# Optimization experiments

Measured on AMD Instinct MI355X. Metric: run time of the kernel, lower is better.

The kernel has to match this reference:

```python
import jax, jax.numpy as jnp
import numpy as np

HIDDEN = 2048
QUANTILES = 16
BATCH = 8192
HALF = HIDDEN // 2


def setup_inputs() -> dict:
    key = jax.random.key(0)
    kx, k1, kb1, k2 = jax.random.split(key, 4)
    x = jax.random.normal(kx, (BATCH, HIDDEN), dtype=jnp.float32)
    # Stacked per-head params: head q computes Linear(H->H/2) -> GELU -> Linear(H/2->1)
    # PyTorch Linear default init ~ U(-1/sqrt(fan_in), 1/sqrt(fan_in)); last layer kaiming-normal, bias 0.
    lim1 = 1.0 / np.sqrt(HIDDEN)
    W1 = jax.random.uniform(k1, (QUANTILES, HIDDEN, HALF), minval=-lim1, maxval=lim1, dtype=jnp.float32)
    b1 = jax.random.uniform(kb1, (QUANTILES, HALF), minval=-lim1, maxval=lim1, dtype=jnp.float32)
    # kaiming_normal fan_in, linear nonlinearity -> std = 1/sqrt(fan_in)
    W2 = jax.random.normal(k2, (QUANTILES, HALF), dtype=jnp.float32) / np.sqrt(HALF)
    b2 = jnp.zeros((QUANTILES,), dtype=jnp.float32)
    return {"x": x, "W1": W1, "b1": b1, "W2": W2, "b2": b2}


def reference(x, W1, b1, W2, b2):
    # Batched over all quantile heads: one grouped GEMM + fused GELU + grouped GEMV.
    # h: [batch, quantiles, half]
    h = jnp.einsum('bh,qhk->bqk', x, W1) + b1[None, :, :]
    h = jax.nn.gelu(h, approximate=False)  # torch nn.GELU() default = exact erf GELU
    # out: [batch, quantiles]
    out = jnp.einsum('bqk,qk->bq', h, W2) + b2[None, :]
    return out
```

## Files before the change

### kernel.cpp

```cpp
#include <hip/hip_runtime.h>

#define HIDDEN 2048
#define QUANT  16
#define BATCH  8192
#define HALFD  1024

typedef _Float16 half8  __attribute__((ext_vector_type(8)));
typedef float    floatx16 __attribute__((ext_vector_type(16)));

__device__ __forceinline__ void load_lds16(const void* gptr, void* lptr) {
  __builtin_amdgcn_global_load_lds(
      (const __attribute__((address_space(1))) void*)gptr,
      (__attribute__((address_space(3))) void*)lptr, 16, 0, 0);
}

__device__ __forceinline__ float gelu_exact(float v) {
  const float z  = 0.7071067811865476f * v;
  const float az = fabsf(z);
  const float t  = __builtin_amdgcn_rcpf(1.0f + 0.3275911f * az);
  const float p  = t * (0.254829592f +
                   t * (-0.284496736f +
                   t * (1.421413741f +
                   t * (-1.453152027f +
                   t * 1.061405429f))));
  float er = 1.0f - p * __expf(-az * az);
  er = copysignf(er, z);
  return 0.5f * v * (1.0f + er);
}

__global__ __launch_bounds__(256) void convert_x_kernel(const float* __restrict__ x,
                                                        _Float16* __restrict__ xh) {
  const int i = (blockIdx.x * 256 + threadIdx.x) * 8;
  const float4 a = *(const float4*)(x + i);
  const float4 b = *(const float4*)(x + i + 4);
  half8 h;
  h[0] = (_Float16)a.x; h[1] = (_Float16)a.y; h[2] = (_Float16)a.z; h[3] = (_Float16)a.w;
  h[4] = (_Float16)b.x; h[5] = (_Float16)b.y; h[6] = (_Float16)b.z; h[7] = (_Float16)b.w;
  *(half8*)(xh + i) = h;
}

__global__ __launch_bounds__(256) void transpose_w1_kernel(const float* __restrict__ W1,
                                                           _Float16* __restrict__ W1T) {
  __shared__ float tile[64][33];
  const int q  = blockIdx.z;
  const int h0 = blockIdx.y * 64;
  const int n0 = blockIdx.x * 32;
  const float* src = W1 + (size_t)q * HIDDEN * HALFD;
  _Float16*    dst = W1T + (size_t)q * HALFD * HIDDEN;
  const int t  = threadIdx.x;
  const int lr = t >> 3;
  const int lc = (t & 7) * 4;
  #pragma unroll
  for (int j = 0; j < 2; ++j) {
    const float4 v = *(const float4*)(src + (size_t)(h0 + lr + 32 * j) * HALFD + n0 + lc);
    tile[lr + 32 * j][lc + 0] = v.x;
    tile[lr + 32 * j][lc + 1] = v.y;
    tile[lr + 32 * j][lc + 2] = v.z;
    tile[lr + 32 * j][lc + 3] = v.w;
  }
  __syncthreads();
  const int sn = t >> 3;
  const int sh = (t & 7) * 8;
  half8 v;
  #pragma unroll
  for (int c = 0; c < 8; ++c) v[c] = (_Float16)tile[sh + c][sn];
  *(half8*)(dst + (size_t)(n0 + sn) * HIDDEN + h0 + sh) = v;
}

__global__ __launch_bounds__(256) void init_out_kernel(float* __restrict__ out,
                                                       const float* __restrict__ b2) {
  const int i = blockIdx.x * 256 + threadIdx.x;
  out[i] = b2[i & (QUANT - 1)];
}

__global__ __launch_bounds__(256, 4) void qhead_gemm_kernel(
    const _Float16* __restrict__ A,
    const _Float16* __restrict__ BT,
    const float* __restrict__ b1,
    const float* __restrict__ W2,
    float* __restrict__ out) {
  __shared__ _Float16 As[128 * 64];
  __shared__ _Float16 Bs[128 * 64];

  const int tid  = threadIdx.x;
  const int lane = tid & 63;
  const int wave = tid >> 6;
  const int wm = wave >> 1, wn = wave & 1;
  const int r31 = lane & 31, l5 = lane >> 5, lx = lane & 7;

  const int m0 = blockIdx.y << 7;
  const int q  = blockIdx.x >> 3;
  const int n0 = (blockIdx.x & 7) << 7;

  const _Float16* Ablk = A + (size_t)m0 * HIDDEN;
  const _Float16* Bblk = BT + ((size_t)q * HALFD + n0) * HIDDEN;

  const int row_t = tid >> 3;
  const int gx = (((tid & 7) ^ (row_t & 7)) << 3);
  const _Float16* agp = Ablk + (size_t)row_t * HIDDEN + gx;
  const _Float16* bgp = Bblk + (size_t)row_t * HIDDEN + gx;
  _Float16* alp = &As[tid * 8];
  _Float16* blp = &Bs[tid * 8];

  int aoff[2], boff[2];
  #pragma unroll
  for (int f = 0; f < 2; ++f) {
    aoff[f] = (wm * 64 + f * 32 + r31) * 64;
    boff[f] = (wn * 64 + f * 32 + r31) * 64;
  }

  floatx16 acc[2][2];
  #pragma unroll
  for (int mf = 0; mf < 2; ++mf)
    #pragma unroll
    for (int nf = 0; nf < 2; ++nf)
      #pragma unroll
      for (int i = 0; i < 16; ++i) acc[mf][nf][i] = 0.f;

  for (int kt = 0; kt < HIDDEN; kt += 64) {
    #pragma unroll
    for (int i = 0; i < 4; ++i)
      load_lds16(agp + (size_t)(i * 32) * HIDDEN + kt, alp + i * 2048);
    #pragma unroll
    for (int i = 0; i < 4; ++i)
      load_lds16(bgp + (size_t)(i * 32) * HIDDEN + kt, blp + i * 2048);
    __syncthreads();

    #pragma unroll
    for (int ks = 0; ks < 4; ++ks) {
      const int p = (((ks << 1) | l5) ^ lx) << 3;
      half8 af[2], bf[2];
      #pragma unroll
      for (int mf = 0; mf < 2; ++mf) af[mf] = *(const half8*)&As[aoff[mf] + p];
      #pragma unroll
      for (int nf = 0; nf < 2; ++nf) bf[nf] = *(const half8*)&Bs[boff[nf] + p];
      #pragma unroll
      for (int mf = 0; mf < 2; ++mf)
        #pragma unroll
        for (int nf = 0; nf < 2; ++nf)
          acc[mf][nf] = __builtin_amdgcn_mfma_f32_32x32x16_f16(af[mf], bf[nf], acc[mf][nf], 0, 0, 0);
    }
    __syncthreads();
  }

  const int nbase = n0 + wn * 64;
  float rowsum[2][16];
  #pragma unroll
  for (int mf = 0; mf < 2; ++mf)
    #pragma unroll
    for (int r = 0; r < 16; ++r) rowsum[mf][r] = 0.f;

  #pragma unroll
  for (int nf = 0; nf < 2; ++nf) {
    const int ncol = nbase + nf * 32 + r31;
    const float b1v = b1[q * HALFD + ncol];
    const float w2v = W2[q * HALFD + ncol];
    #pragma unroll
    for (int mf = 0; mf < 2; ++mf)
      #pragma unroll
      for (int r = 0; r < 16; ++r)
        rowsum[mf][r] += gelu_exact(acc[mf][nf][r] + b1v) * w2v;
  }
  #pragma unroll
  for (int mf = 0; mf < 2; ++mf) {
    #pragma unroll
    for (int r = 0; r < 16; ++r) {
      float t = rowsum[mf][r];
      t += __shfl_xor(t, 1, 64);
      t += __shfl_xor(t, 2, 64);
      t += __shfl_xor(t, 4, 64);
      t += __shfl_xor(t, 8, 64);
      t += __shfl_xor(t, 16, 64);
      rowsum[mf][r] = t;
    }
  }
  if (r31 == 0) {
    #pragma unroll
    for (int mf = 0; mf < 2; ++mf) {
      const int mbase = m0 + wm * 64 + mf * 32 + 4 * l5;
      #pragma unroll
      for (int r = 0; r < 16; ++r) {
        const int mrow = mbase + (r & 3) + 8 * (r >> 2);
        atomicAdd(&out[(size_t)mrow * QUANT + q], rowsum[mf][r]);
      }
    }
  }
}

extern "C" void kernel_launch(void* const* d_in, const int* in_sizes, int n_in,
                              void* d_out, int out_size, void* d_ws, size_t ws_size,
                              hipStream_t stream) {
  const float* x  = (const float*)d_in[0];
  const float* W1 = (const float*)d_in[1];
  const float* b1 = (const float*)d_in[2];
  const float* W2 = (const float*)d_in[3];
  const float* b2 = (const float*)d_in[4];
  float* out = (float*)d_out;

  _Float16* xh  = (_Float16*)d_ws;
  _Float16* w1t = (_Float16*)((char*)d_ws +
                  (size_t)BATCH * HIDDEN * sizeof(_Float16));

  convert_x_kernel<<<BATCH * HIDDEN / (256 * 8), 256, 0, stream>>>(x, xh);
  transpose_w1_kernel<<<dim3(HALFD / 32, HIDDEN / 64, QUANT), 256, 0, stream>>>(W1, w1t);
  init_out_kernel<<<BATCH * QUANT / 256, 256, 0, stream>>>(out, b2);
  qhead_gemm_kernel<<<dim3(128, 64), 256, 0, stream>>>(xh, w1t, b1, W2, out);
}
```

Baseline: 933.2 us.

## Restructure grouped GEMM into 256x256 tiles with 4-stage LDS pipeline

The fused head GEMM now uses 256x256 output tiles with 512 threads and a 4-slot ring of 32-wide K chunks in dynamic LDS. Loads for three stages ahead are issued asynchronously, and a single waitcnt plus barrier per iteration replaces the two full syncthreads. Workgroup IDs are remapped (flat&7 interleave), likely to spread work across XCDs and improve L2 reuse, and MFMA sections raise wave priority. The aim is to hide global-load latency and raise arithmetic intensity per tile. The cost is 128KB of LDS per block and hand-tuned vmcnt accounting that must match exactly.

```diff
diff --git a/kernel.cpp b/kernel.cpp
--- a/kernel.cpp
+++ b/kernel.cpp
@@ -4,6 +4,13 @@
 #define QUANT  16
 #define BATCH  8192
 #define HALFD  1024
+
+#define BM 256
+#define BN 256
+#define BKT 32
+#define NT (HIDDEN / BKT)
+#define A_HALFS (BM * BKT)
+#define SLOT_HALFS (2 * A_HALFS)
 
 typedef _Float16 half8  __attribute__((ext_vector_type(8)));
 typedef float    floatx16 __attribute__((ext_vector_type(16)));
@@ -73,115 +80,119 @@
   out[i] = b2[i & (QUANT - 1)];
 }
 
-__global__ __launch_bounds__(256, 4) void qhead_gemm_kernel(
+__global__ __launch_bounds__(512, 2) void qhead_gemm_kernel(
     const _Float16* __restrict__ A,
     const _Float16* __restrict__ BT,
     const float* __restrict__ b1,
     const float* __restrict__ W2,
     float* __restrict__ out) {
-  __shared__ _Float16 As[128 * 64];
-  __shared__ _Float16 Bs[128 * 64];
+  extern __shared__ _Float16 lds[];
 
   const int tid  = threadIdx.x;
   const int lane = tid & 63;
   const int wave = tid >> 6;
-  const int wm = wave >> 1, wn = wave & 1;
-  const int r31 = lane & 31, l5 = lane >> 5, lx = lane & 7;
-
-  const int m0 = blockIdx.y << 7;
-  const int q  = blockIdx.x >> 3;
-  const int n0 = (blockIdx.x & 7) << 7;
+  const int wm = wave >> 2, wn = wave & 3;
+  const int r31 = lane & 31, l5 = lane >> 5;
+  const int fsw = (r31 >> 1) & 3;
+
+  const int flat = blockIdx.x;
+  const int wg = (flat & 7) * 256 + (flat >> 3);
+  const int mb = wg >> 6;
+  const int qn = wg & 63;
+  const int q  = qn >> 2;
+  const int nb = qn & 3;
+  const int m0 = mb << 8;
 
   const _Float16* Ablk = A + (size_t)m0 * HIDDEN;
-  const _Float16* Bblk = BT + ((size_t)q * HALFD + n0) * HIDDEN;
-
-  const int row_t = tid >> 3;
-  const int gx = (((tid & 7) ^ (row_t & 7)) << 3);
-  const _Float16* agp = Ablk + (size_t)row_t * HIDDEN + gx;
-  const _Float16* bgp = Bblk + (size_t)row_t * HIDDEN + gx;
-  _Float16* alp = &As[tid * 8];
-  _Float16* blp = &Bs[tid * 8];
-
-  int aoff[2], boff[2];
-  #pragma unroll
-  for (int f = 0; f < 2; ++f) {
-    aoff[f] = (wm * 64 + f * 32 + r31) * 64;
-    boff[f] = (wn * 64 + f * 32 + r31) * 64;
-  }
-
-  floatx16 acc[2][2];
-  #pragma unroll
-  for (int mf = 0; mf < 2; ++mf)
+  const _Float16* Bblk = BT + ((size_t)q * HALFD + nb * BN) * HIDDEN;
+
+  const int srow = tid >> 2;
+  const int skg  = (tid & 3) ^ ((srow >> 1) & 3);
+  const _Float16* agp = Ablk + (size_t)srow * HIDDEN + skg * 8;
+  const _Float16* bgp = Bblk + (size_t)srow * HIDDEN + skg * 8;
+
+  int aoff[4], boff[2];
+  #pragma unroll
+  for (int mf = 0; mf < 4; ++mf) aoff[mf] = (wm * 128 + mf * 32 + r31) * BKT;
+  #pragma unroll
+  for (int nf = 0; nf < 2; ++nf) boff[nf] = (wn * 64 + nf * 32 + r31) * BKT + A_HALFS;
+
+  floatx16 acc[4][2];
+  #pragma unroll
+  for (int mf = 0; mf < 4; ++mf)
     #pragma unroll
     for (int nf = 0; nf < 2; ++nf)
       #pragma unroll
       for (int i = 0; i < 16; ++i) acc[mf][nf][i] = 0.f;
 
-  for (int kt = 0; kt < HIDDEN; kt += 64) {
-    #pragma unroll
-    for (int i = 0; i < 4; ++i)
-      load_lds16(agp + (size_t)(i * 32) * HIDDEN + kt, alp + i * 2048);
-    #pragma unroll
-    for (int i = 0; i < 4; ++i)
-      load_lds16(bgp + (size_t)(i * 32) * HIDDEN + kt, blp + i * 2048);
-    __syncthreads();
-
-    #pragma unroll
-    for (int ks = 0; ks < 4; ++ks) {
-      const int p = (((ks << 1) | l5) ^ lx) << 3;
-      half8 af[2], bf[2];
-      #pragma unroll
-      for (int mf = 0; mf < 2; ++mf) af[mf] = *(const half8*)&As[aoff[mf] + p];
-      #pragma unroll
-      for (int nf = 0; nf < 2; ++nf) bf[nf] = *(const half8*)&Bs[boff[nf] + p];
-      #pragma unroll
-      for (int mf = 0; mf < 2; ++mf)
+#define STAGE(ts_) do {                                                    \
+    const int ts = (ts_);                                                  \
+    const int kc = ((ts < NT) ? ts : (ts - NT)) * BKT;   \
+    _Float16* ld = lds + (ts & 3) * SLOT_HALFS + tid * 8;                  \
+    load_lds16(agp + kc, ld);                                              \
+    load_lds16(agp + kc + (size_t)128 * HIDDEN, ld + 4096);                \
+    load_lds16(bgp + kc, ld + A_HALFS);                                    \
+    load_lds16(bgp + kc + (size_t)128 * HIDDEN, ld + A_HALFS + 4096);      \
+  } while (0)
+
+  STAGE(0); STAGE(1); STAGE(2);
+  asm volatile("s_waitcnt vmcnt(8)\n\ts_barrier" ::: "memory");
+
+  #pragma unroll 4
+  for (int t = 0; t < NT; ++t) {
+    STAGE(t + 3);
+    const _Float16* ls = lds + (t & 3) * SLOT_HALFS;
+    __builtin_amdgcn_s_setprio(1);
+    #pragma unroll
+    for (int ks = 0; ks < 2; ++ks) {
+      const int p = (((ks << 1) | l5) ^ fsw) << 3;
+      half8 af[4], bf[2];
+      #pragma unroll
+      for (int mf = 0; mf < 4; ++mf) af[mf] = *(const half8*)(ls + aoff[mf] + p);
+      #pragma unroll
+      for (int nf = 0; nf < 2; ++nf) bf[nf] = *(const half8*)(ls + boff[nf] + p);
+      #pragma unroll
+      for (int mf = 0; mf < 4; ++mf)
         #pragma unroll
         for (int nf = 0; nf < 2; ++nf)
           acc[mf][nf] = __builtin_amdgcn_mfma_f32_32x32x16_f16(af[mf], bf[nf], acc[mf][nf], 0, 0, 0);
     }
-    __syncthreads();
-  }
-
-  const int nbase = n0 + wn * 64;
-  float rowsum[2][16];
-  #pragma unroll
-  for (int mf = 0; mf < 2; ++mf)
-    #pragma unroll
-    for (int r = 0; r < 16; ++r) rowsum[mf][r] = 0.f;
-
-  #pragma unroll
-  for (int nf = 0; nf < 2; ++nf) {
-    const int ncol = nbase + nf * 32 + r31;
-    const float b1v = b1[q * HALFD + ncol];
-    const float w2v = W2[q * HALFD + ncol];
-    #pragma unroll
-    for (int mf = 0; mf < 2; ++mf)
+    __builtin_amdgcn_s_setprio(0);
+    asm volatile("s_waitcnt vmcnt(8) lgkmcnt(0)\n\ts_barrier" ::: "memory");
+  }
+#undef STAGE
+
+  const int colb = nb * BN + wn * 64;
+  #pragma unroll
+  for (int mf = 0; mf < 4; ++mf) {
+    float rs[16];
+    #pragma unroll
+    for (int r = 0; r < 16; ++r) rs[r] = 0.f;
+    #pragma unroll
+    for (int nf = 0; nf < 2; ++nf) {
+      const int ncol = colb + nf * 32 + r31;
+      const float b1v = b1[q * HALFD + ncol];
+      const float w2v = W2[q * HALFD + ncol];
       #pragma unroll
       for (int r = 0; r < 16; ++r)
-        rowsum[mf][r] += gelu_exact(acc[mf][nf][r] + b1v) * w2v;
-  }
-  #pragma unroll
-  for (int mf = 0; mf < 2; ++mf) {
+        rs[r] += gelu_exact(acc[mf][nf][r] + b1v) * w2v;
+    }
     #pragma unroll
     for (int r = 0; r < 16; ++r) {
-      float t = rowsum[mf][r];
-      t += __shfl_xor(t, 1, 64);
-      t += __shfl_xor(t, 2, 64);
-      t += __shfl_xor(t, 4, 64);
-      t += __shfl_xor(t, 8, 64);
-      t += __shfl_xor(t, 16, 64);
-      rowsum[mf][r] = t;
-    }
-  }
-  if (r31 == 0) {
-    #pragma unroll
-    for (int mf = 0; mf < 2; ++mf) {
-      const int mbase = m0 + wm * 64 + mf * 32 + 4 * l5;
+      float v = rs[r];
+      v += __shfl_xor(v, 1, 64);
+      v += __shfl_xor(v, 2, 64);
+      v += __shfl_xor(v, 4, 64);
+      v += __shfl_xor(v, 8, 64);
+      v += __shfl_xor(v, 16, 64);
+      rs[r] = v;
+    }
+    if (r31 == 0) {
+      const int mbase = m0 + wm * 128 + mf * 32 + 4 * l5;
       #pragma unroll
       for (int r = 0; r < 16; ++r) {
         const int mrow = mbase + (r & 3) + 8 * (r >> 2);
-        atomicAdd(&out[(size_t)mrow * QUANT + q], rowsum[mf][r]);
+        atomicAdd(&out[(size_t)mrow * QUANT + q], rs[r]);
       }
     }
   }
@@ -201,8 +212,16 @@
   _Float16* w1t = (_Float16*)((char*)d_ws +
                   (size_t)BATCH * HIDDEN * sizeof(_Float16));
 
+  static int lds_cfg = 0;
+  if (!lds_cfg) {
+    hipFuncSetAttribute(reinterpret_cast<const void*>(qhead_gemm_kernel),
+                        hipFuncAttributeMaxDynamicSharedMemorySize, 131072);
+    lds_cfg = 1;
+  }
+
   convert_x_kernel<<<BATCH * HIDDEN / (256 * 8), 256, 0, stream>>>(x, xh);
   transpose_w1_kernel<<<dim3(HALFD / 32, HIDDEN / 64, QUANT), 256, 0, stream>>>(W1, w1t);
   init_out_kernel<<<BATCH * QUANT / 256, 256, 0, stream>>>(out, b2);
-  qhead_gemm_kernel<<<dim3(128, 64), 256, 0, stream>>>(xh, w1t, b1, W2, out);
-}
+  qhead_gemm_kernel<<<dim3(BATCH / BM * (QUANT * HALFD / BN)), 512, 131072, stream>>>(
+      xh, w1t, b1, W2, out);
+}
```

New measurement: 918.2 us. No clear change (-1.6%).
